# Performance work log

Measured on AMD Instinct MI355X. Metric: run time of the kernel, lower is better.

Reference implementation:

```python
import jax, jax.numpy as jnp
import numpy as np

N = 50000      # nodes
E = 800000     # edges (before self-loops)
F = 128        # input node features
H = 4          # attention heads
C = 32         # per-head channels
HC = H * C     # 128, concat hidden size
LIN = 256
OUT = 10
G = 64         # graphs in batch
NEG_SLOPE = 0.2  # PyG GATConv LeakyReLU default


def setup_inputs() -> dict:
    key = jax.random.key(0)
    ks = jax.random.split(key, 24)
    inp = {
        'x': jax.random.normal(ks[0], (N, F), jnp.float32),
        'edge_index': jax.random.randint(ks[1], (2, E), 0, N, jnp.int64),
        'batch': jnp.sort(jax.random.randint(ks[2], (N,), 0, G, jnp.int64)),
    }
    def w(k, shape, fan_in):
        return jax.random.normal(k, shape, jnp.float32) * (1.0 / np.sqrt(fan_in))
    inp['W0'] = w(ks[3], (F, HC), F)
    inp['as0'] = w(ks[4], (H, C), C)
    inp['ad0'] = w(ks[5], (H, C), C)
    inp['b0'] = jnp.zeros((HC,), jnp.float32)
    inp['W1'] = w(ks[6], (HC, HC), HC)
    inp['as1'] = w(ks[7], (H, C), C)
    inp['ad1'] = w(ks[8], (H, C), C)
    inp['b1'] = jnp.zeros((HC,), jnp.float32)
    inp['W2'] = w(ks[9], (HC, HC), HC)
    inp['as2'] = w(ks[10], (H, C), C)
    inp['ad2'] = w(ks[11], (H, C), C)
    inp['b2'] = jnp.zeros((HC,), jnp.float32)
    inp['Wlin'] = w(ks[12], (HC, LIN), HC)
    inp['blin'] = jnp.zeros((LIN,), jnp.float32)
    inp['Wout'] = w(ks[13], (LIN, OUT), LIN)
    inp['bout'] = jnp.zeros((OUT,), jnp.float32)
    return inp


def gat_conv(x, src, dst, W, a_src, a_dst, b):
    # x: [N, Fin] -> h: [N, H, C]
    n = x.shape[0]
    h = (x @ W).reshape(n, H, C)
    alpha_src = jnp.sum(h * a_src, axis=-1)  # [N, H]
    alpha_dst = jnp.sum(h * a_dst, axis=-1)  # [N, H]
    e = jax.nn.leaky_relu(alpha_src[src] + alpha_dst[dst], NEG_SLOPE)  # [E', H]
    # segment softmax over incoming edges per destination node
    m = jax.ops.segment_max(e, dst, num_segments=n)          # [N, H]
    ex = jnp.exp(e - m[dst])                                 # [E', H]
    denom = jax.ops.segment_sum(ex, dst, num_segments=n)     # [N, H]
    attn = ex / denom[dst]                                   # [E', H]
    out = jax.ops.segment_sum(h[src] * attn[:, :, None], dst, num_segments=n)
    return out.reshape(n, H * C) + b


def reference(x, edge_index, batch, W0, as0, ad0, b0, W1, as1, ad1, b1,
              W2, as2, ad2, b2, Wlin, blin, Wout, bout):
    n = x.shape[0]
    loops = jnp.arange(n, dtype=edge_index.dtype)
    src = jnp.concatenate([edge_index[0], loops])  # PyG add_self_loops=True
    dst = jnp.concatenate([edge_index[1], loops])
    h = jax.nn.relu(gat_conv(x, src, dst, W0, as0, ad0, b0))
    h = jax.nn.relu(gat_conv(h, src, dst, W1, as1, ad1, b1))
    h = jax.nn.relu(gat_conv(h, src, dst, W2, as2, ad2, b2))
    pooled = jax.ops.segment_max(h, batch, num_segments=G)  # global max pool
    pooled = jnp.where(jnp.isfinite(pooled), pooled, 0.0)   # guard empty graphs
    z = pooled @ Wlin + blin
    return z @ Wout + bout
```

## Files before the change

### kernel.cpp

```cpp
#include <hip/hip_runtime.h>
#include <hip/hip_fp16.h>
#include <math.h>

#define N_NODES 50000
#define E_EDGES 800000
#define E_TOT   850000
#define HC 128
#define NHEAD 4
#define LIN 256
#define OUTC 10
#define NG 64
#define NEG_SLOPE 0.2f

__device__ __forceinline__ float lrelu(float v) { return v > 0.f ? v : NEG_SLOPE * v; }

typedef _Float16 half8v __attribute__((ext_vector_type(8)));
typedef float    float4v __attribute__((ext_vector_type(4)));

__global__ __launch_bounds__(256) void k_gemm_mfma(
    const float* __restrict__ x, const float* __restrict__ W,
    const float* __restrict__ a_s, const float* __restrict__ a_d,
    __half* __restrict__ h, float* __restrict__ asrc, float* __restrict__ adst) {
  __shared__ _Float16 Wt[128 * 136];
  __shared__ _Float16 hst[4][16][136];
  __shared__ float aS[HC], aD[HC];
  int tid = threadIdx.x;
  if (tid < HC) { aS[tid] = a_s[tid]; aD[tid] = a_d[tid]; }
  for (int i = 0; i < 64; i++) {
    int idx = tid + i * 256;
    int k = idx >> 7, n = idx & 127;
    Wt[n * 136 + k] = (_Float16)W[idx];
  }
  __syncthreads();

  int wv = tid >> 6, lane = tid & 63;
  int quad = lane >> 4, low = lane & 15;
  int rowbase = blockIdx.x * 64 + wv * 16;
  int row = rowbase + low;
  int rowc = row < N_NODES ? row : N_NODES - 1;

  float4v acc[8];
#pragma unroll
  for (int t = 0; t < 8; t++) acc[t] = (float4v){0.f, 0.f, 0.f, 0.f};

#pragma unroll
  for (int k4 = 0; k4 < 4; k4++) {
    int kb = k4 * 32 + quad * 8;
    float4 xa = *(const float4*)(x + (size_t)rowc * HC + kb);
    float4 xb = *(const float4*)(x + (size_t)rowc * HC + kb + 4);
    half8v af;
    af[0] = (_Float16)xa.x; af[1] = (_Float16)xa.y;
    af[2] = (_Float16)xa.z; af[3] = (_Float16)xa.w;
    af[4] = (_Float16)xb.x; af[5] = (_Float16)xb.y;
    af[6] = (_Float16)xb.z; af[7] = (_Float16)xb.w;
    half8v bf[8];
#pragma unroll
    for (int t = 0; t < 8; t++)
      bf[t] = *(const half8v*)&Wt[(t * 16 + low) * 136 + kb];
#pragma unroll
    for (int t = 0; t < 8; t++)
      acc[t] = __builtin_amdgcn_mfma_f32_16x16x32_f16(af, bf[t], acc[t], 0, 0, 0);
  }

#pragma unroll
  for (int t = 0; t < 8; t++)
#pragma unroll
    for (int r = 0; r < 4; r++)
      hst[wv][quad * 4 + r][t * 16 + low] = (_Float16)acc[t][r];
  __syncthreads();

  {
    int r = lane >> 2, part = lane & 3;
    int grow = rowbase + r;
    if (grow < N_NODES) {
      const float4* src = (const float4*)&hst[wv][r][part * 32];
      float4* dst = (float4*)(h + (size_t)grow * HC + part * 32);
#pragma unroll
      for (int i = 0; i < 4; i++) dst[i] = src[i];
    }
  }
  {
    int grow = rowbase + low;
    float ss = 0.f, dd = 0.f;
#pragma unroll
    for (int i = 0; i < 32; i++) {
      float hv = (float)hst[wv][low][quad * 32 + i];
      ss += hv * aS[quad * 32 + i];
      dd += hv * aD[quad * 32 + i];
    }
    if (grow < N_NODES) {
      asrc[grow * NHEAD + quad] = ss;
      adst[grow * NHEAD + quad] = dd;
    }
  }
}

__global__ __launch_bounds__(256) void k_hist(
    const int* __restrict__ dst, int* __restrict__ deg) {
  int e = blockIdx.x * 256 + threadIdx.x;
  if (e >= E_TOT) return;
  int d = (e < E_EDGES) ? dst[e] : e - E_EDGES;
  atomicAdd(&deg[d], 1);
}

__global__ __launch_bounds__(1024) void k_scan(
    const int* __restrict__ deg, int* __restrict__ row_off,
    unsigned* __restrict__ pooled) {
  if (threadIdx.x < NG * HC / 8) {
    ((uint2*)pooled)[threadIdx.x * 4 + 0] = make_uint2(0u, 0u);
    ((uint2*)pooled)[threadIdx.x * 4 + 1] = make_uint2(0u, 0u);
    ((uint2*)pooled)[threadIdx.x * 4 + 2] = make_uint2(0u, 0u);
    ((uint2*)pooled)[threadIdx.x * 4 + 3] = make_uint2(0u, 0u);
  }
  __shared__ int ps[1024];
  int tid = threadIdx.x;
  const int CH = (N_NODES + 1023) / 1024;
  int base = tid * CH;
  int sum = 0;
  for (int i = 0; i < CH; i++) {
    int idx = base + i;
    if (idx < N_NODES) sum += deg[idx];
  }
  ps[tid] = sum;
  __syncthreads();
  for (int off = 1; off < 1024; off <<= 1) {
    int v = (tid >= off) ? ps[tid - off] : 0;
    __syncthreads();
    ps[tid] += v;
    __syncthreads();
  }
  int run = (tid ? ps[tid - 1] : 0);
  for (int i = 0; i < CH; i++) {
    int idx = base + i;
    if (idx < N_NODES) { row_off[idx] = run; run += deg[idx]; }
  }
  if (tid == 1023) row_off[N_NODES] = run;
}

__global__ __launch_bounds__(256) void k_scatter(
    const int* __restrict__ src, const int* __restrict__ dst,
    const int* __restrict__ row_off, int* __restrict__ cnt,
    int* __restrict__ csr_src) {
  int e = blockIdx.x * 256 + threadIdx.x;
  if (e >= E_TOT) return;
  int s, d;
  if (e < E_EDGES) { s = src[e]; d = dst[e]; } else { s = d = e - E_EDGES; }
  int pos = row_off[d] + atomicAdd(&cnt[d], 1);
  csr_src[pos] = s;
}

#define BFLY_MAX4(m0, m1, m2, m3)                         \
  _Pragma("unroll") for (int off = 1; off < 64; off <<= 1) { \
    m0 = fmaxf(m0, __shfl_xor(m0, off));                  \
    m1 = fmaxf(m1, __shfl_xor(m1, off));                  \
    m2 = fmaxf(m2, __shfl_xor(m2, off));                  \
    m3 = fmaxf(m3, __shfl_xor(m3, off));                  \
  }
#define BFLY_SUM4(s0, s1, s2, s3)                         \
  _Pragma("unroll") for (int off = 1; off < 64; off <<= 1) { \
    s0 += __shfl_xor(s0, off);                            \
    s1 += __shfl_xor(s1, off);                            \
    s2 += __shfl_xor(s2, off);                            \
    s3 += __shfl_xor(s3, off);                            \
  }

__global__ __launch_bounds__(256) void k_aggr(
    const int* __restrict__ row_off, const int* __restrict__ csr_src,
    const float* __restrict__ asrc, const float* __restrict__ adst,
    const __half* __restrict__ h, const float* __restrict__ bias,
    const int* __restrict__ batch, float* __restrict__ out_h,
    unsigned* __restrict__ pooled, int do_pool) {
  __shared__ int   sv_lds[4][64];
  __shared__ float w_lds[4][64][4];
  int gid = blockIdx.x * 256 + threadIdx.x;
  int node = gid >> 6, lane = gid & 63, wl = threadIdx.x >> 6;
  if (node >= N_NODES) return;
  int head = lane >> 4;
  int lo = row_off[node], hi = row_off[node + 1];
  int deg = hi - lo;
  float4 ad4 = ((const float4*)adst)[node];
  float ax = 0.f, ay = 0.f;
  float S;

  if (deg <= 64) {
    int j = lo + lane;
    int sv = (j < hi) ? csr_src[j] : 0;
    float4 a4 = ((const float4*)asrc)[sv];
    bool valid = (j < hi);
    float e0 = valid ? lrelu(a4.x + ad4.x) : -1e30f;
    float e1 = valid ? lrelu(a4.y + ad4.y) : -1e30f;
    float e2 = valid ? lrelu(a4.z + ad4.z) : -1e30f;
    float e3 = valid ? lrelu(a4.w + ad4.w) : -1e30f;
    float m0 = e0, m1 = e1, m2 = e2, m3 = e3;
    BFLY_MAX4(m0, m1, m2, m3)
    float w0 = expf(e0 - m0), w1 = expf(e1 - m1);
    float w2 = expf(e2 - m2), w3 = expf(e3 - m3);
    float s0 = w0, s1 = w1, s2 = w2, s3 = w3;
    BFLY_SUM4(s0, s1, s2, s3)
    sv_lds[wl][lane] = sv;
    *(float4*)&w_lds[wl][lane][0] = make_float4(w0, w1, w2, w3);
    S = (head == 0) ? s0 : (head == 1) ? s1 : (head == 2) ? s2 : s3;
    int jj = 0;
    for (; jj + 8 <= deg; jj += 8) {
      int i0 = sv_lds[wl][jj + 0], i1 = sv_lds[wl][jj + 1];
      int i2 = sv_lds[wl][jj + 2], i3 = sv_lds[wl][jj + 3];
      int i4 = sv_lds[wl][jj + 4], i5 = sv_lds[wl][jj + 5];
      int i6 = sv_lds[wl][jj + 6], i7 = sv_lds[wl][jj + 7];
      float wA = w_lds[wl][jj + 0][head], wB = w_lds[wl][jj + 1][head];
      float wC = w_lds[wl][jj + 2][head], wD = w_lds[wl][jj + 3][head];
      float wE = w_lds[wl][jj + 4][head], wF = w_lds[wl][jj + 5][head];
      float wG = w_lds[wl][jj + 6][head], wH = w_lds[wl][jj + 7][head];
      float2 h0 = __half22float2(*(const __half2*)(h + (size_t)i0 * HC + lane * 2));
      float2 h1 = __half22float2(*(const __half2*)(h + (size_t)i1 * HC + lane * 2));
      float2 h2 = __half22float2(*(const __half2*)(h + (size_t)i2 * HC + lane * 2));
      float2 h3 = __half22float2(*(const __half2*)(h + (size_t)i3 * HC + lane * 2));
      float2 h4 = __half22float2(*(const __half2*)(h + (size_t)i4 * HC + lane * 2));
      float2 h5 = __half22float2(*(const __half2*)(h + (size_t)i5 * HC + lane * 2));
      float2 h6 = __half22float2(*(const __half2*)(h + (size_t)i6 * HC + lane * 2));
      float2 h7 = __half22float2(*(const __half2*)(h + (size_t)i7 * HC + lane * 2));
      ax += wA * h0.x; ay += wA * h0.y;
      ax += wB * h1.x; ay += wB * h1.y;
      ax += wC * h2.x; ay += wC * h2.y;
      ax += wD * h3.x; ay += wD * h3.y;
      ax += wE * h4.x; ay += wE * h4.y;
      ax += wF * h5.x; ay += wF * h5.y;
      ax += wG * h6.x; ay += wG * h6.y;
      ax += wH * h7.x; ay += wH * h7.y;
    }
    for (; jj + 4 <= deg; jj += 4) {
      int i0 = sv_lds[wl][jj + 0], i1 = sv_lds[wl][jj + 1];
      int i2 = sv_lds[wl][jj + 2], i3 = sv_lds[wl][jj + 3];
      float wA = w_lds[wl][jj + 0][head], wB = w_lds[wl][jj + 1][head];
      float wC = w_lds[wl][jj + 2][head], wD = w_lds[wl][jj + 3][head];
      float2 h0 = __half22float2(*(const __half2*)(h + (size_t)i0 * HC + lane * 2));
      float2 h1 = __half22float2(*(const __half2*)(h + (size_t)i1 * HC + lane * 2));
      float2 h2 = __half22float2(*(const __half2*)(h + (size_t)i2 * HC + lane * 2));
      float2 h3 = __half22float2(*(const __half2*)(h + (size_t)i3 * HC + lane * 2));
      ax += wA * h0.x; ay += wA * h0.y;
      ax += wB * h1.x; ay += wB * h1.y;
      ax += wC * h2.x; ay += wC * h2.y;
      ax += wD * h3.x; ay += wD * h3.y;
    }
    for (; jj < deg; jj++) {
      int i0 = sv_lds[wl][jj];
      float wA = w_lds[wl][jj][head];
      float2 h0 = __half22float2(*(const __half2*)(h + (size_t)i0 * HC + lane * 2));
      ax += wA * h0.x; ay += wA * h0.y;
    }
  } else {
    float M0 = -1e30f, M1 = -1e30f, M2 = -1e30f, M3 = -1e30f;
    for (int c = lo; c < hi; c += 64) {
      int j = c + lane;
      int sv = (j < hi) ? csr_src[j] : 0;
      float4 a4 = ((const float4*)asrc)[sv];
      bool valid = (j < hi);
      float e0 = valid ? lrelu(a4.x + ad4.x) : -1e30f;
      float e1 = valid ? lrelu(a4.y + ad4.y) : -1e30f;
      float e2 = valid ? lrelu(a4.z + ad4.z) : -1e30f;
      float e3 = valid ? lrelu(a4.w + ad4.w) : -1e30f;
      BFLY_MAX4(e0, e1, e2, e3)
      M0 = fmaxf(M0, e0); M1 = fmaxf(M1, e1);
      M2 = fmaxf(M2, e2); M3 = fmaxf(M3, e3);
    }
    float S0 = 0.f, S1 = 0.f, S2 = 0.f, S3 = 0.f;
    for (int c = lo; c < hi; c += 64) {
      int j = c + lane;
      int sv = (j < hi) ? csr_src[j] : 0;
      float4 a4 = ((const float4*)asrc)[sv];
      bool valid = (j < hi);
      float e0 = valid ? lrelu(a4.x + ad4.x) : -1e30f;
      float e1 = valid ? lrelu(a4.y + ad4.y) : -1e30f;
      float e2 = valid ? lrelu(a4.z + ad4.z) : -1e30f;
      float e3 = valid ? lrelu(a4.w + ad4.w) : -1e30f;
      float w0 = expf(e0 - M0), w1 = expf(e1 - M1);
      float w2 = expf(e2 - M2), w3 = expf(e3 - M3);
      float s0 = w0, s1 = w1, s2 = w2, s3 = w3;
      BFLY_SUM4(s0, s1, s2, s3)
      S0 += s0; S1 += s1; S2 += s2; S3 += s3;
      sv_lds[wl][lane] = sv;
      *(float4*)&w_lds[wl][lane][0] = make_float4(w0, w1, w2, w3);
      int cnt = (hi - c < 64) ? (hi - c) : 64;
      int jj = 0;
      for (; jj + 4 <= cnt; jj += 4) {
        int i0 = sv_lds[wl][jj + 0], i1 = sv_lds[wl][jj + 1];
        int i2 = sv_lds[wl][jj + 2], i3 = sv_lds[wl][jj + 3];
        float wA = w_lds[wl][jj + 0][head], wB = w_lds[wl][jj + 1][head];
        float wC = w_lds[wl][jj + 2][head], wD = w_lds[wl][jj + 3][head];
        float2 h0 = __half22float2(*(const __half2*)(h + (size_t)i0 * HC + lane * 2));
        float2 h1 = __half22float2(*(const __half2*)(h + (size_t)i1 * HC + lane * 2));
        float2 h2 = __half22float2(*(const __half2*)(h + (size_t)i2 * HC + lane * 2));
        float2 h3 = __half22float2(*(const __half2*)(h + (size_t)i3 * HC + lane * 2));
        ax += wA * h0.x; ay += wA * h0.y;
        ax += wB * h1.x; ay += wB * h1.y;
        ax += wC * h2.x; ay += wC * h2.y;
        ax += wD * h3.x; ay += wD * h3.y;
      }
      for (; jj < cnt; jj++) {
        int i0 = sv_lds[wl][jj];
        float wA = w_lds[wl][jj][head];
        float2 h0 = __half22float2(*(const __half2*)(h + (size_t)i0 * HC + lane * 2));
        ax += wA * h0.x; ay += wA * h0.y;
      }
    }
    S = (head == 0) ? S0 : (head == 1) ? S1 : (head == 2) ? S2 : S3;
  }

  float rden = 1.f / S;
  float2 b = *(const float2*)(bias + lane * 2);
  float vx = fmaxf(ax * rden + b.x, 0.f);
  float vy = fmaxf(ay * rden + b.y, 0.f);
  *(float2*)(out_h + (size_t)node * HC + lane * 2) = make_float2(vx, vy);
  if (do_pool) {
    int g = batch[node];
    unsigned* pp = pooled + g * HC + lane * 2;
    atomicMax(pp + 0, __float_as_uint(vx));
    atomicMax(pp + 1, __float_as_uint(vy));
  }
}

__global__ __launch_bounds__(256) void k_mlp(
    const float* __restrict__ pooled, const float* __restrict__ Wlin,
    const float* __restrict__ blin, const float* __restrict__ Wout,
    const float* __restrict__ bout, float* __restrict__ out) {
  __shared__ float p[HC];
  __shared__ float z[LIN];
  int g = blockIdx.x, tid = threadIdx.x;
  if (tid < HC) p[tid] = pooled[g * HC + tid];
  __syncthreads();
  float zv = blin[tid];
  for (int k = 0; k < HC; k++) zv += p[k] * Wlin[k * LIN + tid];
  z[tid] = zv;
  __syncthreads();
  if (tid < OUTC) {
    float o = bout[tid];
    for (int k = 0; k < LIN; k++) o += z[k] * Wout[k * OUTC + tid];
    out[g * OUTC + tid] = o;
  }
}

extern "C" void kernel_launch(void* const* d_in, const int* in_sizes, int n_in,
                              void* d_out, int out_size, void* d_ws, size_t ws_size,
                              hipStream_t stream) {
  const float* x     = (const float*)d_in[0];
  const int*   ei    = (const int*)d_in[1];
  const int*   batch = (const int*)d_in[2];
  const float* Wl[3] = {(const float*)d_in[3], (const float*)d_in[7], (const float*)d_in[11]};
  const float* As[3] = {(const float*)d_in[4], (const float*)d_in[8], (const float*)d_in[12]};
  const float* Ad[3] = {(const float*)d_in[5], (const float*)d_in[9], (const float*)d_in[13]};
  const float* Bi[3] = {(const float*)d_in[6], (const float*)d_in[10], (const float*)d_in[14]};
  const float* Wlin  = (const float*)d_in[15];
  const float* blin  = (const float*)d_in[16];
  const float* Wout  = (const float*)d_in[17];
  const float* bout  = (const float*)d_in[18];
  float* out = (float*)d_out;

  float* ws = (float*)d_ws;
  __half*   h       = (__half*)ws;
  float*    nodeB   = ws + 6400000;
  float*    asrc    = ws + 12800000;
  float*    adst    = ws + 13000000;
  int*      deg     = (int*)(ws + 13200000);
  int*      cnt     = (int*)(ws + 13250000);
  int*      row_off = (int*)(ws + 13300000);
  int*      csr_src = (int*)(ws + 13350008);
  unsigned* pooled  = (unsigned*)(ws + 14200008);

  const int* srcp = ei;
  const int* dstp = ei + E_EDGES;

  hipMemsetAsync(deg, 0, 2 * N_NODES * sizeof(int), stream);

  k_hist<<<(E_TOT + 255) / 256, 256, 0, stream>>>(dstp, deg);
  k_scan<<<1, 1024, 0, stream>>>(deg, row_off, pooled);
  k_scatter<<<(E_TOT + 255) / 256, 256, 0, stream>>>(srcp, dstp, row_off, cnt, csr_src);

  const float* lin_in = x;
  for (int L = 0; L < 3; L++) {
    k_gemm_mfma<<<(N_NODES + 63) / 64, 256, 0, stream>>>(
        lin_in, Wl[L], As[L], Ad[L], h, asrc, adst);
    k_aggr<<<(N_NODES * 64 + 255) / 256, 256, 0, stream>>>(
        row_off, csr_src, asrc, adst, h, Bi[L], batch,
        nodeB, pooled, (L == 2) ? 1 : 0);
    lin_in = nodeB;
  }
  k_mlp<<<NG, 256, 0, stream>>>((const float*)pooled, Wlin, blin, Wout, bout, out);
}
```

Before: 558.4 us.

## Gather 16-byte feature chunks per lane across four edges in parallel

Restructures the aggregation gather so each wavefront splits into four 16-lane groups. Each group handles a different edge and each lane loads 8 halves (16 bytes) of the source row instead of 4 bytes. Partial sums are then combined across groups with cross-lane shuffles before the bias, ReLU and pooling epilogue. The aim is fewer, wider gather loads and more edges in flight per wavefront. In exchange it adds eight accumulators per lane, a shuffle reduction stage and masked padding work for degrees that are not multiples of 16.

```diff
diff --git a/kernel.cpp b/kernel.cpp
--- a/kernel.cpp
+++ b/kernel.cpp
@@ -175,11 +175,15 @@
   int gid = blockIdx.x * 256 + threadIdx.x;
   int node = gid >> 6, lane = gid & 63, wl = threadIdx.x >> 6;
   if (node >= N_NODES) return;
-  int head = lane >> 4;
+  int g  = lane >> 4;
+  int c  = lane & 15;
+  int hc = c >> 2;
   int lo = row_off[node], hi = row_off[node + 1];
   int deg = hi - lo;
   float4 ad4 = ((const float4*)adst)[node];
-  float ax = 0.f, ay = 0.f;
+  float acc[8];
+#pragma unroll
+  for (int t = 0; t < 8; t++) acc[t] = 0.f;
   float S;
 
   if (deg <= 64) {
@@ -199,58 +203,28 @@
     BFLY_SUM4(s0, s1, s2, s3)
     sv_lds[wl][lane] = sv;
     *(float4*)&w_lds[wl][lane][0] = make_float4(w0, w1, w2, w3);
-    S = (head == 0) ? s0 : (head == 1) ? s1 : (head == 2) ? s2 : s3;
-    int jj = 0;
-    for (; jj + 8 <= deg; jj += 8) {
-      int i0 = sv_lds[wl][jj + 0], i1 = sv_lds[wl][jj + 1];
-      int i2 = sv_lds[wl][jj + 2], i3 = sv_lds[wl][jj + 3];
-      int i4 = sv_lds[wl][jj + 4], i5 = sv_lds[wl][jj + 5];
-      int i6 = sv_lds[wl][jj + 6], i7 = sv_lds[wl][jj + 7];
-      float wA = w_lds[wl][jj + 0][head], wB = w_lds[wl][jj + 1][head];
-      float wC = w_lds[wl][jj + 2][head], wD = w_lds[wl][jj + 3][head];
-      float wE = w_lds[wl][jj + 4][head], wF = w_lds[wl][jj + 5][head];
-      float wG = w_lds[wl][jj + 6][head], wH = w_lds[wl][jj + 7][head];
-      float2 h0 = __half22float2(*(const __half2*)(h + (size_t)i0 * HC + lane * 2));
-      float2 h1 = __half22float2(*(const __half2*)(h + (size_t)i1 * HC + lane * 2));
-      float2 h2 = __half22float2(*(const __half2*)(h + (size_t)i2 * HC + lane * 2));
-      float2 h3 = __half22float2(*(const __half2*)(h + (size_t)i3 * HC + lane * 2));
-      float2 h4 = __half22float2(*(const __half2*)(h + (size_t)i4 * HC + lane * 2));
-      float2 h5 = __half22float2(*(const __half2*)(h + (size_t)i5 * HC + lane * 2));
-      float2 h6 = __half22float2(*(const __half2*)(h + (size_t)i6 * HC + lane * 2));
-      float2 h7 = __half22float2(*(const __half2*)(h + (size_t)i7 * HC + lane * 2));
-      ax += wA * h0.x; ay += wA * h0.y;
-      ax += wB * h1.x; ay += wB * h1.y;
-      ax += wC * h2.x; ay += wC * h2.y;
-      ax += wD * h3.x; ay += wD * h3.y;
-      ax += wE * h4.x; ay += wE * h4.y;
-      ax += wF * h5.x; ay += wF * h5.y;
-      ax += wG * h6.x; ay += wG * h6.y;
-      ax += wH * h7.x; ay += wH * h7.y;
-    }
-    for (; jj + 4 <= deg; jj += 4) {
-      int i0 = sv_lds[wl][jj + 0], i1 = sv_lds[wl][jj + 1];
-      int i2 = sv_lds[wl][jj + 2], i3 = sv_lds[wl][jj + 3];
-      float wA = w_lds[wl][jj + 0][head], wB = w_lds[wl][jj + 1][head];
-      float wC = w_lds[wl][jj + 2][head], wD = w_lds[wl][jj + 3][head];
-      float2 h0 = __half22float2(*(const __half2*)(h + (size_t)i0 * HC + lane * 2));
-      float2 h1 = __half22float2(*(const __half2*)(h + (size_t)i1 * HC + lane * 2));
-      float2 h2 = __half22float2(*(const __half2*)(h + (size_t)i2 * HC + lane * 2));
-      float2 h3 = __half22float2(*(const __half2*)(h + (size_t)i3 * HC + lane * 2));
-      ax += wA * h0.x; ay += wA * h0.y;
-      ax += wB * h1.x; ay += wB * h1.y;
-      ax += wC * h2.x; ay += wC * h2.y;
-      ax += wD * h3.x; ay += wD * h3.y;
-    }
-    for (; jj < deg; jj++) {
-      int i0 = sv_lds[wl][jj];
-      float wA = w_lds[wl][jj][head];
-      float2 h0 = __half22float2(*(const __half2*)(h + (size_t)i0 * HC + lane * 2));
-      ax += wA * h0.x; ay += wA * h0.y;
+    S = (hc == 0) ? s0 : (hc == 1) ? s1 : (hc == 2) ? s2 : s3;
+
+    for (int base = 0; base < deg; base += 16) {
+      float  wv[4];
+      half8v gv[4];
+#pragma unroll
+      for (int u = 0; u < 4; u++) {
+        int jj = base + u * 4 + g;
+        bool val = jj < deg;
+        int svj = sv_lds[wl][val ? jj : 0];
+        wv[u] = val ? w_lds[wl][jj][hc] : 0.f;
+        gv[u] = *(const half8v*)(h + (size_t)svj * HC + c * 8);
+      }
+#pragma unroll
+      for (int u = 0; u < 4; u++)
+#pragma unroll
+        for (int t = 0; t < 8; t++) acc[t] += wv[u] * (float)gv[u][t];
     }
   } else {
     float M0 = -1e30f, M1 = -1e30f, M2 = -1e30f, M3 = -1e30f;
-    for (int c = lo; c < hi; c += 64) {
-      int j = c + lane;
+    for (int cb = lo; cb < hi; cb += 64) {
+      int j = cb + lane;
       int sv = (j < hi) ? csr_src[j] : 0;
       float4 a4 = ((const float4*)asrc)[sv];
       bool valid = (j < hi);
@@ -263,8 +237,8 @@
       M2 = fmaxf(M2, e2); M3 = fmaxf(M3, e3);
     }
     float S0 = 0.f, S1 = 0.f, S2 = 0.f, S3 = 0.f;
-    for (int c = lo; c < hi; c += 64) {
-      int j = c + lane;
+    for (int cb = lo; cb < hi; cb += 64) {
+      int j = cb + lane;
       int sv = (j < hi) ? csr_src[j] : 0;
       float4 a4 = ((const float4*)asrc)[sv];
       bool valid = (j < hi);
@@ -279,40 +253,49 @@
       S0 += s0; S1 += s1; S2 += s2; S3 += s3;
       sv_lds[wl][lane] = sv;
       *(float4*)&w_lds[wl][lane][0] = make_float4(w0, w1, w2, w3);
-      int cnt = (hi - c < 64) ? (hi - c) : 64;
-      int jj = 0;
-      for (; jj + 4 <= cnt; jj += 4) {
-        int i0 = sv_lds[wl][jj + 0], i1 = sv_lds[wl][jj + 1];
-        int i2 = sv_lds[wl][jj + 2], i3 = sv_lds[wl][jj + 3];
-        float wA = w_lds[wl][jj + 0][head], wB = w_lds[wl][jj + 1][head];
-        float wC = w_lds[wl][jj + 2][head], wD = w_lds[wl][jj + 3][head];
-        float2 h0 = __half22float2(*(const __half2*)(h + (size_t)i0 * HC + lane * 2));
-        float2 h1 = __half22float2(*(const __half2*)(h + (size_t)i1 * HC + lane * 2));
-        float2 h2 = __half22float2(*(const __half2*)(h + (size_t)i2 * HC + lane * 2));
-        float2 h3 = __half22float2(*(const __half2*)(h + (size_t)i3 * HC + lane * 2));
-        ax += wA * h0.x; ay += wA * h0.y;
-        ax += wB * h1.x; ay += wB * h1.y;
-        ax += wC * h2.x; ay += wC * h2.y;
-        ax += wD * h3.x; ay += wD * h3.y;
+      int cnt = (hi - cb < 64) ? (hi - cb) : 64;
+      for (int base = 0; base < cnt; base += 16) {
+        float  wv[4];
+        half8v gv[4];
+#pragma unroll
+        for (int u = 0; u < 4; u++) {
+          int jj = base + u * 4 + g;
+          bool val = jj < cnt;
+          int svj = sv_lds[wl][val ? jj : 0];
+          wv[u] = val ? w_lds[wl][jj][hc] : 0.f;
+          gv[u] = *(const half8v*)(h + (size_t)svj * HC + c * 8);
+        }
+#pragma unroll
+        for (int u = 0; u < 4; u++)
+#pragma unroll
+          for (int t = 0; t < 8; t++) acc[t] += wv[u] * (float)gv[u][t];
       }
-      for (; jj < cnt; jj++) {
-        int i0 = sv_lds[wl][jj];
-        float wA = w_lds[wl][jj][head];
-        float2 h0 = __half22float2(*(const __half2*)(h + (size_t)i0 * HC + lane * 2));
-        ax += wA * h0.x; ay += wA * h0.y;
-      }
-    }
-    S = (head == 0) ? S0 : (head == 1) ? S1 : (head == 2) ? S2 : S3;
-  }
+    }
+    S = (hc == 0) ? S0 : (hc == 1) ? S1 : (hc == 2) ? S2 : S3;
+  }
+
+#pragma unroll
+  for (int off = 16; off < 64; off <<= 1)
+#pragma unroll
+    for (int t = 0; t < 8; t++) acc[t] += __shfl_xor(acc[t], off);
 
   float rden = 1.f / S;
-  float2 b = *(const float2*)(bias + lane * 2);
-  float vx = fmaxf(ax * rden + b.x, 0.f);
-  float vy = fmaxf(ay * rden + b.y, 0.f);
-  *(float2*)(out_h + (size_t)node * HC + lane * 2) = make_float2(vx, vy);
+  float4 b0 = *(const float4*)(bias + c * 8);
+  float4 b1 = *(const float4*)(bias + c * 8 + 4);
+  float v0 = fmaxf(acc[0] * rden + b0.x, 0.f);
+  float v1 = fmaxf(acc[1] * rden + b0.y, 0.f);
+  float v2 = fmaxf(acc[2] * rden + b0.z, 0.f);
+  float v3 = fmaxf(acc[3] * rden + b0.w, 0.f);
+  float v4 = fmaxf(acc[4] * rden + b1.x, 0.f);
+  float v5 = fmaxf(acc[5] * rden + b1.y, 0.f);
+  float v6 = fmaxf(acc[6] * rden + b1.z, 0.f);
+  float v7 = fmaxf(acc[7] * rden + b1.w, 0.f);
+  float vx = (g == 0) ? v0 : (g == 1) ? v2 : (g == 2) ? v4 : v6;
+  float vy = (g == 0) ? v1 : (g == 1) ? v3 : (g == 2) ? v5 : v7;
+  *(float2*)(out_h + (size_t)node * HC + c * 8 + 2 * g) = make_float2(vx, vy);
   if (do_pool) {
-    int g = batch[node];
-    unsigned* pp = pooled + g * HC + lane * 2;
+    int gb = batch[node];
+    unsigned* pp = pooled + gb * HC + c * 8 + 2 * g;
     atomicMax(pp + 0, __float_as_uint(vx));
     atomicMax(pp + 1, __float_as_uint(vy));
   }
```

Result: slower. 607.9 us (+8.9%).

## Bucket CSR edges by source tile and replace single-block scan with multi-block scan

Applied to the files above, without the earlier changes.

Each destination's incoming edge list is now sub-sorted into five source-node tiles, so gathers of source features during aggregation touch rows in rough order and may get better cache locality. Building this needs a five-times larger histogram (N*NT). The old single-block scan is therefore replaced with a three-kernel multi-block scan (reduce, scan the block sums, then per-block scan). The price is more atomics spread over more counters, two extra launches, and larger workspace offsets that were rearranged. The h buffer region also shrinks to match an fp16 size.

```diff
diff --git a/kernel.cpp b/kernel.cpp
--- a/kernel.cpp
+++ b/kernel.cpp
@@ -11,6 +11,11 @@
 #define OUTC 10
 #define NG 64
 #define NEG_SLOPE 0.2f
+
+#define NT 5
+#define TILE_N 10000
+#define NSEG (N_NODES * NT)
+#define SCAN_BLOCKS 245
 
 __device__ __forceinline__ float lrelu(float v) { return v > 0.f ? v : NEG_SLOPE * v; }
 
@@ -96,56 +101,102 @@
 }
 
 __global__ __launch_bounds__(256) void k_hist(
-    const int* __restrict__ dst, int* __restrict__ deg) {
+    const int* __restrict__ dst, const int* __restrict__ src,
+    int* __restrict__ degT) {
   int e = blockIdx.x * 256 + threadIdx.x;
   if (e >= E_TOT) return;
-  int d = (e < E_EDGES) ? dst[e] : e - E_EDGES;
-  atomicAdd(&deg[d], 1);
-}
-
-__global__ __launch_bounds__(1024) void k_scan(
-    const int* __restrict__ deg, int* __restrict__ row_off,
+  int d, s;
+  if (e < E_EDGES) { d = dst[e]; s = src[e]; } else { d = s = e - E_EDGES; }
+  int t = s / TILE_N;
+  atomicAdd(&degT[d * NT + t], 1);
+}
+
+__global__ __launch_bounds__(256) void k_scanA(
+    const int* __restrict__ degT, int* __restrict__ bsum) {
+  __shared__ int ps[256];
+  int tid = threadIdx.x, b = blockIdx.x;
+  int base = b * 1024 + tid * 4;
+  int s = 0;
+#pragma unroll
+  for (int i = 0; i < 4; i++) {
+    int idx = base + i;
+    if (idx < NSEG) s += degT[idx];
+  }
+  ps[tid] = s;
+  __syncthreads();
+  for (int off = 128; off > 0; off >>= 1) {
+    if (tid < off) ps[tid] += ps[tid + off];
+    __syncthreads();
+  }
+  if (tid == 0) bsum[b] = ps[0];
+}
+
+__global__ __launch_bounds__(256) void k_scanB(
+    const int* __restrict__ bsum, int* __restrict__ boff,
     unsigned* __restrict__ pooled) {
-  if (threadIdx.x < NG * HC / 8) {
-    ((uint2*)pooled)[threadIdx.x * 4 + 0] = make_uint2(0u, 0u);
-    ((uint2*)pooled)[threadIdx.x * 4 + 1] = make_uint2(0u, 0u);
-    ((uint2*)pooled)[threadIdx.x * 4 + 2] = make_uint2(0u, 0u);
-    ((uint2*)pooled)[threadIdx.x * 4 + 3] = make_uint2(0u, 0u);
-  }
-  __shared__ int ps[1024];
+  __shared__ int ps[256];
   int tid = threadIdx.x;
-  const int CH = (N_NODES + 1023) / 1024;
-  int base = tid * CH;
-  int sum = 0;
-  for (int i = 0; i < CH; i++) {
-    int idx = base + i;
-    if (idx < N_NODES) sum += deg[idx];
-  }
-  ps[tid] = sum;
-  __syncthreads();
-  for (int off = 1; off < 1024; off <<= 1) {
+  {
+    uint4* p4 = (uint4*)pooled;
+#pragma unroll
+    for (int i = 0; i < 8; i++) p4[tid * 8 + i] = make_uint4(0u, 0u, 0u, 0u);
+  }
+  int s = (tid < SCAN_BLOCKS) ? bsum[tid] : 0;
+  ps[tid] = s;
+  __syncthreads();
+  for (int off = 1; off < 256; off <<= 1) {
     int v = (tid >= off) ? ps[tid - off] : 0;
     __syncthreads();
     ps[tid] += v;
     __syncthreads();
   }
-  int run = (tid ? ps[tid - 1] : 0);
-  for (int i = 0; i < CH; i++) {
+  if (tid < SCAN_BLOCKS) boff[tid] = ps[tid] - s;
+}
+
+__global__ __launch_bounds__(256) void k_scanC(
+    const int* __restrict__ degT, const int* __restrict__ boff,
+    int* __restrict__ offT) {
+  __shared__ int ps[256];
+  int tid = threadIdx.x, b = blockIdx.x;
+  int base = b * 1024 + tid * 4;
+  int d[4];
+  int s = 0;
+#pragma unroll
+  for (int i = 0; i < 4; i++) {
     int idx = base + i;
-    if (idx < N_NODES) { row_off[idx] = run; run += deg[idx]; }
-  }
-  if (tid == 1023) row_off[N_NODES] = run;
+    d[i] = (idx < NSEG) ? degT[idx] : 0;
+    s += d[i];
+  }
+  ps[tid] = s;
+  __syncthreads();
+  for (int off = 1; off < 256; off <<= 1) {
+    int v = (tid >= off) ? ps[tid - off] : 0;
+    __syncthreads();
+    ps[tid] += v;
+    __syncthreads();
+  }
+  int run = boff[b] + ps[tid] - s;
+#pragma unroll
+  for (int i = 0; i < 4; i++) {
+    int idx = base + i;
+    if (idx < NSEG) {
+      offT[idx] = run;
+      run += d[i];
+      if (idx == NSEG - 1) offT[NSEG] = run;
+    }
+  }
 }
 
 __global__ __launch_bounds__(256) void k_scatter(
     const int* __restrict__ src, const int* __restrict__ dst,
-    const int* __restrict__ row_off, int* __restrict__ cnt,
+    const int* __restrict__ offT, int* __restrict__ cntT,
     int* __restrict__ csr_src) {
   int e = blockIdx.x * 256 + threadIdx.x;
   if (e >= E_TOT) return;
   int s, d;
   if (e < E_EDGES) { s = src[e]; d = dst[e]; } else { s = d = e - E_EDGES; }
-  int pos = row_off[d] + atomicAdd(&cnt[d], 1);
+  int t = s / TILE_N;
+  int pos = offT[d * NT + t] + atomicAdd(&cntT[d * NT + t], 1);
   csr_src[pos] = s;
 }
 
@@ -165,7 +216,7 @@
   }
 
 __global__ __launch_bounds__(256) void k_aggr(
-    const int* __restrict__ row_off, const int* __restrict__ csr_src,
+    const int* __restrict__ offT, const int* __restrict__ csr_src,
     const float* __restrict__ asrc, const float* __restrict__ adst,
     const __half* __restrict__ h, const float* __restrict__ bias,
     const int* __restrict__ batch, float* __restrict__ out_h,
@@ -176,7 +227,7 @@
   int node = gid >> 6, lane = gid & 63, wl = threadIdx.x >> 6;
   if (node >= N_NODES) return;
   int head = lane >> 4;
-  int lo = row_off[node], hi = row_off[node + 1];
+  int lo = offT[node * NT], hi = offT[node * NT + NT];
   int deg = hi - lo;
   float4 ad4 = ((const float4*)adst)[node];
   float ax = 0.f, ay = 0.f;
@@ -356,30 +407,34 @@
 
   float* ws = (float*)d_ws;
   __half*   h       = (__half*)ws;
-  float*    nodeB   = ws + 6400000;
-  float*    asrc    = ws + 12800000;
-  float*    adst    = ws + 13000000;
-  int*      deg     = (int*)(ws + 13200000);
-  int*      cnt     = (int*)(ws + 13250000);
-  int*      row_off = (int*)(ws + 13300000);
-  int*      csr_src = (int*)(ws + 13350008);
-  unsigned* pooled  = (unsigned*)(ws + 14200008);
+  float*    nodeB   = ws + 3200000;
+  float*    asrc    = ws + 9600000;
+  float*    adst    = ws + 9800000;
+  int*      degT    = (int*)(ws + 10000000);
+  int*      cntT    = (int*)(ws + 10250000);
+  int*      offT    = (int*)(ws + 10500000);
+  int*      csr_src = (int*)(ws + 10750004);
+  unsigned* pooled  = (unsigned*)(ws + 11600008);
+  int*      bsum    = (int*)(ws + 11608200);
+  int*      boff    = (int*)(ws + 11608456);
 
   const int* srcp = ei;
   const int* dstp = ei + E_EDGES;
 
-  hipMemsetAsync(deg, 0, 2 * N_NODES * sizeof(int), stream);
-
-  k_hist<<<(E_TOT + 255) / 256, 256, 0, stream>>>(dstp, deg);
-  k_scan<<<1, 1024, 0, stream>>>(deg, row_off, pooled);
-  k_scatter<<<(E_TOT + 255) / 256, 256, 0, stream>>>(srcp, dstp, row_off, cnt, csr_src);
+  hipMemsetAsync(degT, 0, 2 * NSEG * sizeof(int), stream);
+
+  k_hist<<<(E_TOT + 255) / 256, 256, 0, stream>>>(dstp, srcp, degT);
+  k_scanA<<<SCAN_BLOCKS, 256, 0, stream>>>(degT, bsum);
+  k_scanB<<<1, 256, 0, stream>>>(bsum, boff, pooled);
+  k_scanC<<<SCAN_BLOCKS, 256, 0, stream>>>(degT, boff, offT);
+  k_scatter<<<(E_TOT + 255) / 256, 256, 0, stream>>>(srcp, dstp, offT, cntT, csr_src);
 
   const float* lin_in = x;
   for (int L = 0; L < 3; L++) {
     k_gemm_mfma<<<(N_NODES + 63) / 64, 256, 0, stream>>>(
         lin_in, Wl[L], As[L], Ad[L], h, asrc, adst);
     k_aggr<<<(N_NODES * 64 + 255) / 256, 256, 0, stream>>>(
-        row_off, csr_src, asrc, adst, h, Bi[L], batch,
+        offT, csr_src, asrc, adst, h, Bi[L], batch,
         nodeB, pooled, (L == 2) ? 1 : 0);
     lin_in = nodeB;
   }
```

After: 508.3 us. 1.1x faster.
